# Kernel optimization log

Measured on AMD Instinct MI355X. Metric: run time of the kernel, lower is better.

Reference implementation:

```python
import jax, jax.numpy as jnp
import numpy as np

N_NODES = 100000
N_EDGES = 3200000
IN_DIM = 128
OUT_DIM = 128


def setup_inputs() -> dict:
    key = jax.random.key(0)
    k1, k2, k3, k4, k5 = jax.random.split(key, 5)
    fea_input = jax.random.normal(k1, (N_NODES, IN_DIM), dtype=jnp.float32)
    edge_row = jax.random.randint(k2, (N_EDGES,), 0, N_NODES, dtype=jnp.int32)
    edge_col = jax.random.randint(k3, (N_EDGES,), 0, N_NODES, dtype=jnp.int32)
    edge_val = jax.random.uniform(k4, (N_EDGES,), dtype=jnp.float32)
    # kaiming_uniform-style init for weight, zeros for bias
    bound = float(np.sqrt(6.0 / IN_DIM))
    weight = jax.random.uniform(k5, (IN_DIM, OUT_DIM), dtype=jnp.float32,
                                minval=-bound, maxval=bound)
    bias = jnp.zeros((OUT_DIM,), dtype=jnp.float32)
    return {
        "fea_input": fea_input,
        "edge_row": edge_row,
        "edge_col": edge_col,
        "edge_val": edge_val,
        "weight": weight,
        "bias": bias,
    }


def reference(fea_input, edge_row, edge_col, edge_val, weight, bias):
    # support = X @ W  -> [N, OUT_DIM]
    support = jnp.matmul(fea_input, weight)
    # SpMM: out[r] += val * support[c] for each edge (r, c, val)
    gathered = support[edge_col] * edge_val[:, None]  # [E, OUT_DIM]
    output = jax.ops.segment_sum(gathered, edge_row, num_segments=N_NODES)
    return output + bias
```

## Files before the change

### kernel.cpp

```cpp
#include <hip/hip_runtime.h>
#include <hip/hip_bf16.h>


#define N_NODES 100000
#define N_EDGES 3200000
#define DIM 128
#define RB 16
#define RPB 128
#define NBKT ((N_NODES + RPB - 1) / RPB)
#define CHUNK 8192
#define NCHK ((N_EDGES + CHUNK - 1) / CHUNK)
#define CAP 6016

typedef __attribute__((ext_vector_type(8))) short bf16x8;
typedef __attribute__((ext_vector_type(4))) float f32x4;
typedef unsigned long long u64;
typedef unsigned int u32;

__device__ inline ushort bf16rne(float f) {
  uint32_t u = __float_as_uint(f);
  u += 0x7fffu + ((u >> 16) & 1u);
  return (ushort)(u >> 16);
}

__global__ __launch_bounds__(256) void prep_count_kernel(
    const float* __restrict__ X, const float* __restrict__ W,
    ushort* __restrict__ Xh, ushort* __restrict__ Wh,
    const int* __restrict__ erow, int* __restrict__ bcnt,
    int* __restrict__ table) {
  __shared__ int cnt[NBKT];
  if (blockIdx.x < 1024) {
    const size_t nx4 = (size_t)N_NODES * DIM / 4;
    const size_t nw4 = (size_t)DIM * DIM / 4;
    for (size_t i = (size_t)blockIdx.x * blockDim.x + threadIdx.x;
         i < nx4 + nw4; i += (size_t)1024 * blockDim.x) {
      const float4 f = (i < nx4) ? ((const float4*)X)[i] : ((const float4*)W)[i - nx4];
      ushort4 h;
      h.x = bf16rne(f.x); h.y = bf16rne(f.y); h.z = bf16rne(f.z); h.w = bf16rne(f.w);
      if (i < nx4) ((ushort4*)Xh)[i] = h;
      else         ((ushort4*)Wh)[i - nx4] = h;
    }
  } else {
    const int cb = blockIdx.x - 1024;
    for (int b = threadIdx.x; b < NBKT; b += 256) cnt[b] = 0;
    __syncthreads();
    const int e0 = cb * CHUNK;
    #pragma unroll
    for (int it = 0; it < CHUNK / 256; ++it) {
      const int e = e0 + it * 256 + threadIdx.x;
      if (e < N_EDGES) atomicAdd(&cnt[erow[e] >> 7], 1);
    }
    __syncthreads();
    for (int b = threadIdx.x; b < NBKT; b += 256) {
      const int c = cnt[b];
      table[(size_t)cb * NBKT + b] = c;
      if (c) atomicAdd(&bcnt[b], c);
    }
  }
}

__global__ __launch_bounds__(1024) void bscan_kernel(int* __restrict__ bcur,
                                                     int* __restrict__ bbase) {
  __shared__ int wsum[16];
  const int t = threadIdx.x, lane = t & 63, wid = t >> 6;
  const int v = (t < NBKT) ? bcur[t] : 0;
  int incl = v;
  #pragma unroll
  for (int off = 1; off < 64; off <<= 1) {
    int n = __shfl_up(incl, off, 64);
    if (lane >= off) incl += n;
  }
  if (lane == 63) wsum[wid] = incl;
  __syncthreads();
  if (t == 0) {
    int s = 0;
    #pragma unroll
    for (int w = 0; w < 16; ++w) { int x = wsum[w]; wsum[w] = s; s += x; }
  }
  __syncthreads();
  const int excl = wsum[wid] + incl - v;
  if (t < NBKT) { bbase[t] = excl; bcur[t] = excl; }
  if (t == NBKT - 1) bbase[NBKT] = excl + v;
}

__global__ __launch_bounds__(256) void partition_kernel(
    const int* __restrict__ erow, const int* __restrict__ ecol,
    const float* __restrict__ eval, const int* __restrict__ table,
    int* __restrict__ bcur, u64* __restrict__ p64) {
  __shared__ int cnt[NBKT];
  const int e0 = blockIdx.x * CHUNK;
  for (int b = threadIdx.x; b < NBKT; b += 256) {
    const int c = table[(size_t)blockIdx.x * NBKT + b];
    cnt[b] = c ? atomicAdd(&bcur[b], c) : 0;
  }
  __syncthreads();
  #pragma unroll
  for (int it = 0; it < CHUNK / 256; ++it) {
    const int e = e0 + it * 256 + threadIdx.x;
    if (e < N_EDGES) {
      const int r = erow[e];
      const u32 lo = ((u32)ecol[e] << 15) | (u32)bf16rne(eval[e]);
      const int p = atomicAdd(&cnt[r >> 7], 1);
      p64[p] = ((u64)(r & (RPB - 1)) << 32) | (u64)lo;
    }
  }
}

__global__ __launch_bounds__(256) void bsort_kernel(
    const int* __restrict__ bbase, u64* __restrict__ p64,
    int* __restrict__ row_ptr, ushort* __restrict__ row_len) {
  __shared__ u64 ebuf[CAP];
  __shared__ int hist[RPB];
  __shared__ int excl[RPB];
  __shared__ int wtot;
  const int b = blockIdx.x, t = threadIdx.x;
  const int s = bbase[b];
  int nE = bbase[b + 1] - s;
  if (nE > CAP) nE = CAP;
  const u64* src = p64 + s;
  for (int i = t; i < nE; i += 256) ebuf[i] = src[i];
  if (t < RPB) hist[t] = 0;
  __syncthreads();
  for (int i = t; i < nE; i += 256)
    atomicAdd(&hist[(int)(ebuf[i] >> 32) & (RPB - 1)], 1);
  __syncthreads();
  int v = 0, incl = 0;
  if (t < RPB) {
    v = hist[t];
    incl = v;
    #pragma unroll
    for (int off = 1; off < 64; off <<= 1) {
      int n = __shfl_up(incl, off, 64);
      if ((t & 63) >= off) incl += n;
    }
    if (t == 63) wtot = incl;
  }
  __syncthreads();
  if (t < RPB) {
    const int e = incl - v + ((t >= 64) ? wtot : 0);
    excl[t] = e;
    const int gr = b * RPB + t;
    if (gr < N_NODES) { row_ptr[gr] = s + e; row_len[gr] = (ushort)v; }
  }
  __syncthreads();
  for (int i = t; i < nE; i += 256) {
    const u64 w = ebuf[i];
    const int p = atomicAdd(&excl[(int)(w >> 32) & (RPB - 1)], 1);
    const u32 lo = (u32)w;
    const u32 off = (lo >> 7) & 0xFFFFFF00u;
    const u32 vb  = (lo & 0x7fffu) << 16;
    p64[s + p] = ((u64)vb << 32) | (u64)off;
  }
}

__global__ __launch_bounds__(256) void agg_kernel(
    const ushort* __restrict__ Xh,
    const int* __restrict__ row_ptr, const ushort* __restrict__ row_len,
    const u64* __restrict__ edges, ushort* __restrict__ Yh) {
  const int r = blockIdx.x * 4 + (threadIdx.x >> 6);
  if (r >= N_NODES) return;
  const int lane = threadIdx.x & 63;
  const u32 lane4 = (u32)lane * 4u;
  const char* Xb = (const char*)Xh;
  const int s0 = row_ptr[r];
  const int s1 = s0 + (int)row_len[r];
  float ax0 = 0.f, ay0 = 0.f, ax1 = 0.f, ay1 = 0.f;
  float ax2 = 0.f, ay2 = 0.f, ax3 = 0.f, ay3 = 0.f;
  int e = s0;
  if ((e & 1) && e < s1) {
    const u64 w = edges[e];
    const float v = __uint_as_float((u32)(w >> 32));
    const u32 q = *(const u32*)(Xb + ((u32)w + lane4));
    ax0 += v * __uint_as_float(q << 16);
    ay0 += v * __uint_as_float(q & 0xffff0000u);
    ++e;
  }
  for (; e + 8 <= s1; e += 8) {
    const uint4 pa = *(const uint4*)(edges + e);
    const uint4 pb = *(const uint4*)(edges + e + 2);
    const uint4 pc = *(const uint4*)(edges + e + 4);
    const uint4 pd = *(const uint4*)(edges + e + 6);
    const u32 q0 = *(const u32*)(Xb + (pa.x + lane4));
    const u32 q1 = *(const u32*)(Xb + (pa.z + lane4));
    const u32 q2 = *(const u32*)(Xb + (pb.x + lane4));
    const u32 q3 = *(const u32*)(Xb + (pb.z + lane4));
    const u32 q4 = *(const u32*)(Xb + (pc.x + lane4));
    const u32 q5 = *(const u32*)(Xb + (pc.z + lane4));
    const u32 q6 = *(const u32*)(Xb + (pd.x + lane4));
    const u32 q7 = *(const u32*)(Xb + (pd.z + lane4));
    const float v0 = __uint_as_float(pa.y), v1 = __uint_as_float(pa.w);
    const float v2 = __uint_as_float(pb.y), v3 = __uint_as_float(pb.w);
    const float v4 = __uint_as_float(pc.y), v5 = __uint_as_float(pc.w);
    const float v6 = __uint_as_float(pd.y), v7 = __uint_as_float(pd.w);
    ax0 += v0 * __uint_as_float(q0 << 16);
    ay0 += v0 * __uint_as_float(q0 & 0xffff0000u);
    ax1 += v1 * __uint_as_float(q1 << 16);
    ay1 += v1 * __uint_as_float(q1 & 0xffff0000u);
    ax2 += v2 * __uint_as_float(q2 << 16);
    ay2 += v2 * __uint_as_float(q2 & 0xffff0000u);
    ax3 += v3 * __uint_as_float(q3 << 16);
    ay3 += v3 * __uint_as_float(q3 & 0xffff0000u);
    ax0 += v4 * __uint_as_float(q4 << 16);
    ay0 += v4 * __uint_as_float(q4 & 0xffff0000u);
    ax1 += v5 * __uint_as_float(q5 << 16);
    ay1 += v5 * __uint_as_float(q5 & 0xffff0000u);
    ax2 += v6 * __uint_as_float(q6 << 16);
    ay2 += v6 * __uint_as_float(q6 & 0xffff0000u);
    ax3 += v7 * __uint_as_float(q7 << 16);
    ay3 += v7 * __uint_as_float(q7 & 0xffff0000u);
  }
  for (; e + 2 <= s1; e += 2) {
    const uint4 p = *(const uint4*)(edges + e);
    const u32 qa = *(const u32*)(Xb + (p.x + lane4));
    const u32 qb = *(const u32*)(Xb + (p.z + lane4));
    const float va = __uint_as_float(p.y), vb = __uint_as_float(p.w);
    ax0 += va * __uint_as_float(qa << 16);
    ay0 += va * __uint_as_float(qa & 0xffff0000u);
    ax1 += vb * __uint_as_float(qb << 16);
    ay1 += vb * __uint_as_float(qb & 0xffff0000u);
  }
  if (e < s1) {
    const u64 w = edges[e];
    const float v = __uint_as_float((u32)(w >> 32));
    const u32 q = *(const u32*)(Xb + ((u32)w + lane4));
    ax0 += v * __uint_as_float(q << 16);
    ay0 += v * __uint_as_float(q & 0xffff0000u);
  }
  const float ax = (ax0 + ax1) + (ax2 + ax3);
  const float ay = (ay0 + ay1) + (ay2 + ay3);
  const u32 py = (u32)bf16rne(ax) | ((u32)bf16rne(ay) << 16);
  ((u32*)(Yh + (size_t)r * DIM))[lane] = py;
}

__global__ __launch_bounds__(256) void gemm_mfma(const ushort* __restrict__ Yh,
                                                 const ushort* __restrict__ Wh,
                                                 const float* __restrict__ bias,
                                                 float* __restrict__ out) {
  const int wid = threadIdx.x >> 6, lane = threadIdx.x & 63;
  const int lr = lane & 15, lq = lane >> 4;
  const int n0 = wid * 32;

  bf16x8 bfrag[4][2];
  float bval[2];
  #pragma unroll
  for (int nt = 0; nt < 2; ++nt) {
    const int col = n0 + nt * 16 + lr;
    bval[nt] = bias[col];
    #pragma unroll
    for (int kk = 0; kk < 4; ++kk) {
      const int kbase = kk * 32 + lq * 8;
      bf16x8 b;
      #pragma unroll
      for (int i = 0; i < 8; ++i)
        b[i] = (short)Wh[(size_t)(kbase + i) * DIM + col];
      bfrag[kk][nt] = b;
    }
  }

  const int r0 = blockIdx.x * 256;
  #pragma unroll 1
  for (int g = 0; g < 16; ++g) {
    const int m0 = r0 + g * 16;
    if (m0 >= N_NODES) break;
    bf16x8 afrag[4];
    const ushort* arow = Yh + (size_t)(m0 + lr) * DIM + lq * 8;
    #pragma unroll
    for (int kk = 0; kk < 4; ++kk)
      afrag[kk] = *(const bf16x8*)(arow + kk * 32);
    #pragma unroll
    for (int nt = 0; nt < 2; ++nt) {
      f32x4 acc = {0.f, 0.f, 0.f, 0.f};
      #pragma unroll
      for (int kk = 0; kk < 4; ++kk)
        acc = __builtin_amdgcn_mfma_f32_16x16x32_bf16(afrag[kk], bfrag[kk][nt], acc, 0, 0, 0);
      const int col = n0 + nt * 16 + lr;
      #pragma unroll
      for (int j = 0; j < 4; ++j)
        out[(size_t)(m0 + lq * 4 + j) * DIM + col] = acc[j] + bval[nt];
    }
  }
}

__global__ __launch_bounds__(128) void gemm_kernel(
    const float* __restrict__ IN, const float* __restrict__ W,
    float* __restrict__ OUT, const float* __restrict__ bias, int add_bias) {
  __shared__ float Wsh[DIM * DIM];
  __shared__ float Xsh[RB * DIM];
  const int t = threadIdx.x;
  #pragma unroll 8
  for (int i = 0; i < DIM; ++i) Wsh[i * DIM + t] = W[i * DIM + t];
  const int r0 = blockIdx.x * RB;
  #pragma unroll
  for (int idx = t; idx < RB * DIM; idx += 128)
    Xsh[idx] = IN[(size_t)r0 * DIM + idx];
  __syncthreads();
  float acc[RB];
  const float b = add_bias ? bias[t] : 0.f;
  #pragma unroll
  for (int r = 0; r < RB; ++r) acc[r] = b;
  for (int k = 0; k < DIM; ++k) {
    const float w = Wsh[k * DIM + t];
    #pragma unroll
    for (int r = 0; r < RB; ++r) acc[r] += Xsh[r * DIM + k] * w;
  }
  #pragma unroll
  for (int r = 0; r < RB; ++r)
    OUT[(size_t)(r0 + r) * DIM + t] = acc[r];
}

__global__ void init_kernel(float* __restrict__ out, const float* __restrict__ bias) {
  const size_t total4 = (size_t)N_NODES * DIM / 4;
  const float4* b4 = (const float4*)bias;
  float4* o4 = (float4*)out;
  for (size_t i = (size_t)blockIdx.x * blockDim.x + threadIdx.x;
       i < total4; i += (size_t)gridDim.x * blockDim.x)
    o4[i] = b4[i & 31];
}

__global__ __launch_bounds__(256) void scatter_kernel(
    const float* __restrict__ S,
    const int* __restrict__ erow, const int* __restrict__ ecol,
    const float* __restrict__ eval, float* __restrict__ out) {
  const long long g = (long long)blockIdx.x * blockDim.x + threadIdx.x;
  const long long e = g >> 5;
  const int lane = (int)(g & 31);
  if (e >= N_EDGES) return;
  const int r = erow[e];
  const int c = ecol[e];
  const float v = eval[e];
  const float4 x = ((const float4*)(S + (size_t)c * DIM))[lane];
  float* o = out + (size_t)r * DIM + lane * 4;
  atomicAdd(o + 0, v * x.x);
  atomicAdd(o + 1, v * x.y);
  atomicAdd(o + 2, v * x.z);
  atomicAdd(o + 3, v * x.w);
}

extern "C" void kernel_launch(void* const* d_in, const int* in_sizes, int n_in,
                              void* d_out, int out_size, void* d_ws, size_t ws_size,
                              hipStream_t stream) {
  const float* X    = (const float*)d_in[0];
  const int*   erow = (const int*)d_in[1];
  const int*   ecol = (const int*)d_in[2];
  const float* eval = (const float*)d_in[3];
  const float* W    = (const float*)d_in[4];
  const float* bias = (const float*)d_in[5];
  float* out = (float*)d_out;

  const size_t P64_BYTES = (size_t)N_EDGES * 8;
  const size_t XH_BYTES  = (size_t)N_NODES * DIM * 2;
  const size_t YH_BYTES  = (size_t)N_NODES * DIM * 2;
  const size_t WH_BYTES  = (size_t)DIM * DIM * 2;
  const size_t RP_BYTES  = (size_t)N_NODES * 4;
  const size_t RL_BYTES  = (size_t)N_NODES * 2;
  const size_t BB_BYTES  = (size_t)(NBKT + 1) * 4;
  const size_t BC_BYTES  = (size_t)NBKT * 4;
  const size_t NEED = P64_BYTES + XH_BYTES + YH_BYTES + WH_BYTES +
                      RP_BYTES + RL_BYTES + BB_BYTES + BC_BYTES + 256;

  if (ws_size >= NEED) {
    char* w = (char*)d_ws;
    u64*    p64     = (u64*)w;     w += P64_BYTES;
    ushort* Xh      = (ushort*)w;  w += XH_BYTES;
    ushort* Yh      = (ushort*)w;  w += YH_BYTES;
    ushort* Wh      = (ushort*)w;  w += WH_BYTES;
    int*    row_ptr = (int*)w;     w += RP_BYTES;
    ushort* row_len = (ushort*)w;  w += RL_BYTES;
    int*    bbase   = (int*)w;     w += BB_BYTES;
    int*    bcur    = (int*)w;
    int*    table   = (int*)Yh;

    hipMemsetAsync(bcur, 0, BC_BYTES, stream);
    prep_count_kernel<<<1024 + NCHK, 256, 0, stream>>>(X, W, Xh, Wh, erow, bcur, table);
    bscan_kernel<<<1, 1024, 0, stream>>>(bcur, bbase);
    partition_kernel<<<NCHK, 256, 0, stream>>>(erow, ecol, eval, table, bcur, p64);
    bsort_kernel<<<NBKT, 256, 0, stream>>>(bbase, p64, row_ptr, row_len);
    agg_kernel<<<(N_NODES + 3) / 4, 256, 0, stream>>>(Xh, row_ptr, row_len, p64, Yh);
    gemm_mfma<<<(N_NODES + 255) / 256, 256, 0, stream>>>(Yh, Wh, bias, out);
  } else {
    float* S = (float*)d_ws;
    init_kernel<<<2048, 256, 0, stream>>>(out, bias);
    gemm_kernel<<<N_NODES / RB, 128, 0, stream>>>(X, W, S, bias, 0);
    const long long threads = (long long)N_EDGES * 32;
    scatter_kernel<<<(int)((threads + 255) / 256), 256, 0, stream>>>(S, erow, ecol, eval, out);
  }
}
```

Baseline: 248.1 us.

## Split each row's edges across four lane groups with 16-byte gathers

```diff
diff --git a/kernel.cpp b/kernel.cpp
--- a/kernel.cpp
+++ b/kernel.cpp
@@ -22,6 +22,8 @@
   u += 0x7fffu + ((u >> 16) & 1u);
   return (ushort)(u >> 16);
 }
+__device__ inline float lofl(u32 u) { return __uint_as_float(u << 16); }
+__device__ inline float hifl(u32 u) { return __uint_as_float(u & 0xffff0000u); }
 
 __global__ __launch_bounds__(256) void prep_count_kernel(
     const float* __restrict__ X, const float* __restrict__ W,
@@ -160,76 +162,59 @@
   const int r = blockIdx.x * 4 + (threadIdx.x >> 6);
   if (r >= N_NODES) return;
   const int lane = threadIdx.x & 63;
-  const u32 lane4 = (u32)lane * 4u;
+  const int q = lane >> 4;
+  const u32 sub16 = (u32)(lane & 15) * 16u;
   const char* Xb = (const char*)Xh;
   const int s0 = row_ptr[r];
   const int s1 = s0 + (int)row_len[r];
-  float ax0 = 0.f, ay0 = 0.f, ax1 = 0.f, ay1 = 0.f;
-  float ax2 = 0.f, ay2 = 0.f, ax3 = 0.f, ay3 = 0.f;
-  int e = s0;
-  if ((e & 1) && e < s1) {
-    const u64 w = edges[e];
-    const float v = __uint_as_float((u32)(w >> 32));
-    const u32 q = *(const u32*)(Xb + ((u32)w + lane4));
-    ax0 += v * __uint_as_float(q << 16);
-    ay0 += v * __uint_as_float(q & 0xffff0000u);
-    ++e;
-  }
-  for (; e + 8 <= s1; e += 8) {
-    const uint4 pa = *(const uint4*)(edges + e);
-    const uint4 pb = *(const uint4*)(edges + e + 2);
-    const uint4 pc = *(const uint4*)(edges + e + 4);
-    const uint4 pd = *(const uint4*)(edges + e + 6);
-    const u32 q0 = *(const u32*)(Xb + (pa.x + lane4));
-    const u32 q1 = *(const u32*)(Xb + (pa.z + lane4));
-    const u32 q2 = *(const u32*)(Xb + (pb.x + lane4));
-    const u32 q3 = *(const u32*)(Xb + (pb.z + lane4));
-    const u32 q4 = *(const u32*)(Xb + (pc.x + lane4));
-    const u32 q5 = *(const u32*)(Xb + (pc.z + lane4));
-    const u32 q6 = *(const u32*)(Xb + (pd.x + lane4));
-    const u32 q7 = *(const u32*)(Xb + (pd.z + lane4));
-    const float v0 = __uint_as_float(pa.y), v1 = __uint_as_float(pa.w);
-    const float v2 = __uint_as_float(pb.y), v3 = __uint_as_float(pb.w);
-    const float v4 = __uint_as_float(pc.y), v5 = __uint_as_float(pc.w);
-    const float v6 = __uint_as_float(pd.y), v7 = __uint_as_float(pd.w);
-    ax0 += v0 * __uint_as_float(q0 << 16);
-    ay0 += v0 * __uint_as_float(q0 & 0xffff0000u);
-    ax1 += v1 * __uint_as_float(q1 << 16);
-    ay1 += v1 * __uint_as_float(q1 & 0xffff0000u);
-    ax2 += v2 * __uint_as_float(q2 << 16);
-    ay2 += v2 * __uint_as_float(q2 & 0xffff0000u);
-    ax3 += v3 * __uint_as_float(q3 << 16);
-    ay3 += v3 * __uint_as_float(q3 & 0xffff0000u);
-    ax0 += v4 * __uint_as_float(q4 << 16);
-    ay0 += v4 * __uint_as_float(q4 & 0xffff0000u);
-    ax1 += v5 * __uint_as_float(q5 << 16);
-    ay1 += v5 * __uint_as_float(q5 & 0xffff0000u);
-    ax2 += v6 * __uint_as_float(q6 << 16);
-    ay2 += v6 * __uint_as_float(q6 & 0xffff0000u);
-    ax3 += v7 * __uint_as_float(q7 << 16);
-    ay3 += v7 * __uint_as_float(q7 & 0xffff0000u);
-  }
-  for (; e + 2 <= s1; e += 2) {
-    const uint4 p = *(const uint4*)(edges + e);
-    const u32 qa = *(const u32*)(Xb + (p.x + lane4));
-    const u32 qb = *(const u32*)(Xb + (p.z + lane4));
-    const float va = __uint_as_float(p.y), vb = __uint_as_float(p.w);
-    ax0 += va * __uint_as_float(qa << 16);
-    ay0 += va * __uint_as_float(qa & 0xffff0000u);
-    ax1 += vb * __uint_as_float(qb << 16);
-    ay1 += vb * __uint_as_float(qb & 0xffff0000u);
-  }
-  if (e < s1) {
-    const u64 w = edges[e];
-    const float v = __uint_as_float((u32)(w >> 32));
-    const u32 q = *(const u32*)(Xb + ((u32)w + lane4));
-    ax0 += v * __uint_as_float(q << 16);
-    ay0 += v * __uint_as_float(q & 0xffff0000u);
-  }
-  const float ax = (ax0 + ax1) + (ax2 + ax3);
-  const float ay = (ay0 + ay1) + (ay2 + ay3);
-  const u32 py = (u32)bf16rne(ax) | ((u32)bf16rne(ay) << 16);
-  ((u32*)(Yh + (size_t)r * DIM))[lane] = py;
+  float f0 = 0.f, f1 = 0.f, f2 = 0.f, f3 = 0.f;
+  float f4 = 0.f, f5 = 0.f, f6 = 0.f, f7 = 0.f;
+  for (int e = s0 + q; e < s1 || (e - q) < s1; e += 16) {
+    const u64 w0 = (e      < s1) ? edges[e]      : 0ull;
+    const u64 w1 = (e + 4  < s1) ? edges[e + 4]  : 0ull;
+    const u64 w2 = (e + 8  < s1) ? edges[e + 8]  : 0ull;
+    const u64 w3 = (e + 12 < s1) ? edges[e + 12] : 0ull;
+    const uint4 g0 = *(const uint4*)(Xb + ((u32)w0 + sub16));
+    const uint4 g1 = *(const uint4*)(Xb + ((u32)w1 + sub16));
+    const uint4 g2 = *(const uint4*)(Xb + ((u32)w2 + sub16));
+    const uint4 g3 = *(const uint4*)(Xb + ((u32)w3 + sub16));
+    const float v0 = __uint_as_float((u32)(w0 >> 32));
+    const float v1 = __uint_as_float((u32)(w1 >> 32));
+    const float v2 = __uint_as_float((u32)(w2 >> 32));
+    const float v3 = __uint_as_float((u32)(w3 >> 32));
+    f0 += v0 * lofl(g0.x); f1 += v0 * hifl(g0.x);
+    f2 += v0 * lofl(g0.y); f3 += v0 * hifl(g0.y);
+    f4 += v0 * lofl(g0.z); f5 += v0 * hifl(g0.z);
+    f6 += v0 * lofl(g0.w); f7 += v0 * hifl(g0.w);
+    f0 += v1 * lofl(g1.x); f1 += v1 * hifl(g1.x);
+    f2 += v1 * lofl(g1.y); f3 += v1 * hifl(g1.y);
+    f4 += v1 * lofl(g1.z); f5 += v1 * hifl(g1.z);
+    f6 += v1 * lofl(g1.w); f7 += v1 * hifl(g1.w);
+    f0 += v2 * lofl(g2.x); f1 += v2 * hifl(g2.x);
+    f2 += v2 * lofl(g2.y); f3 += v2 * hifl(g2.y);
+    f4 += v2 * lofl(g2.z); f5 += v2 * hifl(g2.z);
+    f6 += v2 * lofl(g2.w); f7 += v2 * hifl(g2.w);
+    f0 += v3 * lofl(g3.x); f1 += v3 * hifl(g3.x);
+    f2 += v3 * lofl(g3.y); f3 += v3 * hifl(g3.y);
+    f4 += v3 * lofl(g3.z); f5 += v3 * hifl(g3.z);
+    f6 += v3 * lofl(g3.w); f7 += v3 * hifl(g3.w);
+  }
+  f0 += __shfl_xor(f0, 16); f1 += __shfl_xor(f1, 16);
+  f2 += __shfl_xor(f2, 16); f3 += __shfl_xor(f3, 16);
+  f4 += __shfl_xor(f4, 16); f5 += __shfl_xor(f5, 16);
+  f6 += __shfl_xor(f6, 16); f7 += __shfl_xor(f7, 16);
+  f0 += __shfl_xor(f0, 32); f1 += __shfl_xor(f1, 32);
+  f2 += __shfl_xor(f2, 32); f3 += __shfl_xor(f3, 32);
+  f4 += __shfl_xor(f4, 32); f5 += __shfl_xor(f5, 32);
+  f6 += __shfl_xor(f6, 32); f7 += __shfl_xor(f7, 32);
+  if (lane < 16) {
+    uint4 o;
+    o.x = (u32)bf16rne(f0) | ((u32)bf16rne(f1) << 16);
+    o.y = (u32)bf16rne(f2) | ((u32)bf16rne(f3) << 16);
+    o.z = (u32)bf16rne(f4) | ((u32)bf16rne(f5) << 16);
+    o.w = (u32)bf16rne(f6) | ((u32)bf16rne(f7) << 16);
+    ((uint4*)(Yh + (size_t)r * DIM))[lane] = o;
+  }
 }
 
 __global__ __launch_bounds__(256) void gemm_mfma(const ushort* __restrict__ Yh,
```

Measured after the change: 242.6 us. -2.2%, faster.
